# Kernel tuning notes

Measured on AMD Instinct MI355X. Metric: run time of the kernel, lower is better.

Reference implementation:

```python
import jax, jax.numpy as jnp
import numpy as np

B, N, E = 4, 4096, 1024
H, D = 16, 64          # num_heads, head_dim
K = 256                # proj_dim
MAXN = 4096
RANK = 32


def setup_inputs() -> dict:
    key = jax.random.key(0)
    ks = jax.random.split(key, 9)
    def w(k, shape, fan_in):
        return jax.random.normal(k, shape, jnp.float32) * (1.0 / np.sqrt(fan_in))
    return {
        "x": jax.random.normal(ks[0], (B, N, E), jnp.float32),
        "qU": w(ks[1], (RANK, E), E),            # LowRankLinear U: [rank, in]
        "qV": w(ks[2], (E // 2, RANK), RANK),    # LowRankLinear V: [out, rank]
        "qW": w(ks[3], (H * D, E // 2), E // 2), # final query Linear weight
        "qb": jnp.zeros((H * D,), jnp.float32),
        "kW": w(ks[4], (D, E), E),               # key_transform (single kv head)
        "key_proj": w(ks[5], (MAXN, K), MAXN),   # Linformer projection [max_seq_len, proj_dim]
        "oW": w(ks[6], (E, H * D), H * D),
        "ob": jnp.zeros((E,), jnp.float32),
    }


def reference(x, qU, qV, qW, qb, kW, key_proj, oW, ob):
    b, n, _ = x.shape
    # query: LowRankLinear then Linear
    q = ((x @ qU.T) @ qV.T) @ qW.T + qb              # [b, n, H*D]
    # shared single-head key/value, projected along sequence to K slots
    k = x @ kW.T                                     # [b, n, D]
    kv = jnp.einsum('bnd,nk->bkd', k, key_proj[:n])  # [b, K, D]
    q = q.reshape(b, n, H, D).transpose(0, 2, 1, 3)  # [b, H, n, D]
    kv = kv[:, None]                                 # [b, 1, K, D] broadcasts over heads
    scores = jnp.einsum('bhnd,bhkd->bhnk', q, kv) * (D ** -0.5)
    w = jax.nn.softmax(scores, axis=-1)              # [b, H, n, K]
    out = jnp.einsum('bhnk,bhkd->bhnd', w, kv)       # [b, H, n, D]
    out = out.transpose(0, 2, 1, 3).reshape(b, n, H * D)
    return out @ oW.T + ob
```

## Files before the change

### kernel.cpp

```cpp
#include <hip/hip_runtime.h>


typedef unsigned short u16;
typedef _Float16 f16;
typedef __attribute__((ext_vector_type(8))) _Float16 h8;
typedef __attribute__((ext_vector_type(4))) float f32x4;
typedef __attribute__((ext_vector_type(8))) unsigned short us8;
typedef __attribute__((ext_vector_type(4))) unsigned short us4;

__device__ __forceinline__ u16 f2h(float x) {
    f16 h = (f16)x;
    union { f16 hf; u16 u; } c; c.hf = h; return c.u;
}
__device__ __forceinline__ void async16(const void* g, void* l) {
    __builtin_amdgcn_global_load_lds(
        (const __attribute__((address_space(1))) void*)g,
        (__attribute__((address_space(3))) void*)l, 16, 0, 0);
}

__global__ __launch_bounds__(256)
void cvt_w(const float* __restrict__ src, u16* __restrict__ h, int n4) {
    int i = blockIdx.x * 256 + threadIdx.x;
    if (i >= n4) return;
    float4 v = ((const float4*)src)[i];
    u16 hh[4] = {f2h(v.x), f2h(v.y), f2h(v.z), f2h(v.w)};
    ((us4*)h)[i] = *(const us4*)hh;
}

template <bool HAS_BIAS, bool OUT_F16>
__global__ __launch_bounds__(256)
void gemm_ps(const u16* __restrict__ A_g, const u16* __restrict__ B_g,
             const float* __restrict__ bias, void* __restrict__ C_p,
             int M, int N, int K) {
    __shared__ u16 LA[128 * 32], LB[128 * 32];
    const int t = threadIdx.x;
    const int wave = t >> 6, lane = t & 63;
    const int l15 = lane & 15, quad = lane >> 4;
    const int wm = (wave >> 1) * 64, wn = (wave & 1) * 64;
    const int gx = gridDim.x;
    const int nwg = gx * gridDim.y;
    const int flat = blockIdx.y * gx + blockIdx.x;
    const int cpx = nwg >> 3;
    const int swz = (flat & 7) * cpx + (flat >> 3);
    const int m0 = (swz / gx) * 128, n0 = (swz % gx) * 128;
    const int rl = lane >> 2, c4 = lane & 3;

    f32x4 acc[4][4] = {};

    for (int k0 = 0; k0 < K; k0 += 32) {
#pragma unroll
        for (int j = 0; j < 2; ++j) {
            const int rloc = (wave * 2 + j) * 16 + rl;
            const size_t ga = (size_t)(m0 + rloc) * K + k0 + c4 * 8;
            const size_t gb = (size_t)(n0 + rloc) * K + k0 + c4 * 8;
            const int lo = (wave * 2 + j) * 512;
            async16(&A_g[ga], &LA[lo]);
            async16(&B_g[gb], &LB[lo]);
        }
        __syncthreads();

        h8 ah[4], bh[4];
#pragma unroll
        for (int i = 0; i < 4; ++i) {
            ah[i] = *(const h8*)&LA[(wm + i * 16 + l15) * 32 + quad * 8];
            bh[i] = *(const h8*)&LB[(wn + i * 16 + l15) * 32 + quad * 8];
        }
#pragma unroll
        for (int i = 0; i < 4; ++i)
#pragma unroll
            for (int j = 0; j < 4; ++j)
                acc[i][j] = __builtin_amdgcn_mfma_f32_16x16x32_f16(ah[i], bh[j], acc[i][j], 0, 0, 0);
        __syncthreads();
    }

#pragma unroll
    for (int j = 0; j < 4; ++j) {
        const int col = n0 + wn + j * 16 + l15;
        const float badd = HAS_BIAS ? bias[col] : 0.f;
#pragma unroll
        for (int i = 0; i < 4; ++i) {
            const int rbase = m0 + wm + i * 16 + quad * 4;
#pragma unroll
            for (int r = 0; r < 4; ++r) {
                float v = acc[i][j][r] + badd;
                size_t idx = (size_t)(rbase + r) * N + col;
                if (OUT_F16) ((u16*)C_p)[idx] = f2h(v);
                else         ((float*)C_p)[idx] = v;
            }
        }
    }
}

template <int BN, bool OUT_F16>
__global__ __launch_bounds__(256)
void gemm_xa(const float* __restrict__ A, const u16* __restrict__ B_g,
             void* __restrict__ C_p, int M, int N, int K) {
    constexpr int MI = (BN == 128) ? 4 : 2;
    constexpr int NJ = (BN == 32) ? 2 : 4;
    __shared__ u16 Ah[128][40], Bh[BN][40];
    const int t = threadIdx.x;
    const int wave = t >> 6, lane = t & 63;
    const int l15 = lane & 15, quad = lane >> 4;
    const int wm = (BN == 128) ? (wave >> 1) * 64 : wave * 32;
    const int wn = (BN == 128) ? (wave & 1) * 64 : 0;
    const int m0 = blockIdx.y * 128, n0 = blockIdx.x * BN;
    const int arow = t >> 1, acol = (t & 1) * 16;

    f32x4 acc[MI][NJ] = {};

    for (int k0 = 0; k0 < K; k0 += 32) {
        {
            const float* src = &A[(size_t)(m0 + arow) * K + k0 + acol];
            float4 w0 = ((const float4*)src)[0], w1 = ((const float4*)src)[1];
            float4 w2 = ((const float4*)src)[2], w3 = ((const float4*)src)[3];
            float v[16] = {w0.x, w0.y, w0.z, w0.w, w1.x, w1.y, w1.z, w1.w,
                           w2.x, w2.y, w2.z, w2.w, w3.x, w3.y, w3.z, w3.w};
            u16 hh[16];
#pragma unroll
            for (int e = 0; e < 16; ++e) hh[e] = f2h(v[e]);
            *(us8*)&Ah[arow][acol]     = *(const us8*)&hh[0];
            *(us8*)&Ah[arow][acol + 8] = *(const us8*)&hh[8];
        }
        if (t < BN * 2) {
            const int brow = t >> 1, bcol = (t & 1) * 16;
            size_t base = (size_t)(n0 + brow) * K + k0 + bcol;
            *(us8*)&Bh[brow][bcol]     = *(const us8*)&B_g[base];
            *(us8*)&Bh[brow][bcol + 8] = *(const us8*)&B_g[base + 8];
        }
        __syncthreads();

        h8 ah[MI], bh[NJ];
#pragma unroll
        for (int i = 0; i < MI; ++i)
            ah[i] = *(const h8*)&Ah[wm + i * 16 + l15][quad * 8];
#pragma unroll
        for (int j = 0; j < NJ; ++j)
            bh[j] = *(const h8*)&Bh[wn + j * 16 + l15][quad * 8];
#pragma unroll
        for (int i = 0; i < MI; ++i)
#pragma unroll
            for (int j = 0; j < NJ; ++j)
                acc[i][j] = __builtin_amdgcn_mfma_f32_16x16x32_f16(ah[i], bh[j], acc[i][j], 0, 0, 0);
        __syncthreads();
    }

#pragma unroll
    for (int j = 0; j < NJ; ++j) {
        const int col = n0 + wn + j * 16 + l15;
#pragma unroll
        for (int i = 0; i < MI; ++i) {
            const int rbase = m0 + wm + i * 16 + quad * 4;
#pragma unroll
            for (int r = 0; r < 4; ++r) {
                float v = acc[i][j][r];
                size_t idx = (size_t)(rbase + r) * N + col;
                if (OUT_F16) ((u16*)C_p)[idx] = f2h(v);
                else         ((float*)C_p)[idx] = v;
            }
        }
    }
}

__global__ __launch_bounds__(256)
void kv_partial(const float* __restrict__ kmat, const float* __restrict__ kp,
                float* __restrict__ part) {
    const int b = blockIdx.y;
    const int seg = blockIdx.z;
    const int kk0 = blockIdx.x * 16;
    const int tid = threadIdx.x;
    const int d = tid & 63, s = tid >> 6;

    float acc[16] = {};
    const int nbeg = seg * 512;
    for (int n = nbeg + s; n < nbeg + 512; n += 4) {
        const float kval = kmat[((size_t)b * 4096 + n) * 64 + d];
        const float* kpr = &kp[(size_t)n * 256 + kk0];
#pragma unroll
        for (int j = 0; j < 16; ++j) acc[j] += kval * kpr[j];
    }
    __shared__ float sm[16][4][64];
#pragma unroll
    for (int j = 0; j < 16; ++j) sm[j][s][d] = acc[j];
    __syncthreads();
    for (int o = tid; o < 16 * 64; o += 256) {
        const int j = o >> 6, dd = o & 63;
        part[(((size_t)seg * 4 + b) * 256 + kk0 + j) * 64 + dd] =
            sm[j][0][dd] + sm[j][1][dd] + sm[j][2][dd] + sm[j][3][dd];
    }
}

__global__ __launch_bounds__(256)
void kv_reduce_cvt(const float* __restrict__ part,
                   u16* __restrict__ kvh, u16* __restrict__ kvTh) {
    const int i = blockIdx.x * 256 + threadIdx.x;
    float s = 0.f;
#pragma unroll
    for (int seg = 0; seg < 8; ++seg) s += part[(size_t)seg * 65536 + i];
    u16 hh = f2h(s);
    kvh[i] = hh;
    const int b = i >> 14, k = (i >> 6) & 255, d = i & 63;
    kvTh[((size_t)b * 64 + d) * 256 + k] = hh;
}

__global__ __launch_bounds__(256)
void attn_fused(const u16* __restrict__ qh,
                const u16* __restrict__ kvh, const u16* __restrict__ kvTh,
                u16* __restrict__ ath) {
    __shared__ u16 Kh_s[64][72];
    __shared__ u16 Vh_s[64][72];
    __shared__ u16 Ps[128 * 64];
    const int b = blockIdx.z, h = blockIdx.y;
    const int t = threadIdx.x, wave = t >> 6, lane = t & 63;
    const int l15 = lane & 15, quad = lane >> 4;
    const int nblk = blockIdx.x * 128;
    const int nwav = wave * 32;
    char* Pb = (char*)Ps;

    h8 Qf[2][2];
#pragma unroll
    for (int nt = 0; nt < 2; ++nt) {
        size_t qoff = ((size_t)(b * 4096 + nblk + nwav + nt * 16 + l15)) * 1024
                      + h * 64 + quad * 8;
#pragma unroll
        for (int c = 0; c < 2; ++c)
            Qf[nt][c] = *(const h8*)&qh[qoff + c * 32];
    }

    f32x4 O[2][4] = {};
    float rsum[2] = {0.f, 0.f};

    const int srow = t >> 3;
    const int scol = (t & 7) * 8;
    const size_t kb = (size_t)b * 16384;

    for (int kc = 0; kc < 4; ++kc) {
        {
            us8 s0 = *(const us8*)&kvh [kb + (size_t)(kc * 64 + srow     ) * 64 + scol];
            us8 s1 = *(const us8*)&kvh [kb + (size_t)(kc * 64 + srow + 32) * 64 + scol];
            us8 s4 = *(const us8*)&kvTh[kb + (size_t)(srow     ) * 256 + kc * 64 + scol];
            us8 s5 = *(const us8*)&kvTh[kb + (size_t)(srow + 32) * 256 + kc * 64 + scol];
            *(us8*)&Kh_s[srow     ][scol] = s0;
            *(us8*)&Kh_s[srow + 32][scol] = s1;
            *(us8*)&Vh_s[srow     ][scol] = s4;
            *(us8*)&Vh_s[srow + 32][scol] = s5;
        }
        __syncthreads();

        f32x4 S[2][4] = {};
#pragma unroll
        for (int ktl = 0; ktl < 4; ++ktl) {
            const int krl = ktl * 16 + l15;
#pragma unroll
            for (int c = 0; c < 2; ++c) {
                h8 Kf = *(const h8*)&Kh_s[krl][c * 32 + quad * 8];
#pragma unroll
                for (int nt = 0; nt < 2; ++nt)
                    S[nt][ktl] = __builtin_amdgcn_mfma_f32_16x16x32_f16(Kf, Qf[nt][c], S[nt][ktl], 0, 0, 0);
            }
        }
#pragma unroll
        for (int nt = 0; nt < 2; ++nt) {
            const int nrel = nwav + nt * 16 + l15;
#pragma unroll
            for (int ktl = 0; ktl < 4; ++ktl) {
                u16 pw[4];
#pragma unroll
                for (int r = 0; r < 4; ++r) {
                    float p = __expf(S[nt][ktl][r] * 0.125f - 4.0f);
                    rsum[nt] += p;
                    pw[r] = f2h(p);
                }
                *(us4*)(Pb + ((nrel * 128 + ktl * 32 + quad * 8) ^ ((nrel & 7) << 4)))
                    = *(const us4*)pw;
            }
        }

#pragma unroll
        for (int c = 0; c < 2; ++c) {
            h8 pf[2];
#pragma unroll
            for (int nt = 0; nt < 2; ++nt) {
                const int nrel = nwav + nt * 16 + l15;
                pf[nt] = *(const h8*)(Pb + ((nrel * 128 + c * 64 + quad * 16) ^ ((nrel & 7) << 4)));
            }
#pragma unroll
            for (int dt = 0; dt < 4; ++dt) {
                const int drow = dt * 16 + l15;
                h8 th = *(const h8*)&Vh_s[drow][c * 32 + quad * 8];
#pragma unroll
                for (int nt = 0; nt < 2; ++nt)
                    O[nt][dt] = __builtin_amdgcn_mfma_f32_16x16x32_f16(pf[nt], th, O[nt][dt], 0, 0, 0);
            }
        }
        __syncthreads();
    }

    float inv[2];
#pragma unroll
    for (int nt = 0; nt < 2; ++nt) {
        float s = rsum[nt];
        s += __shfl_xor(s, 16, 64);
        s += __shfl_xor(s, 32, 64);
        inv[nt] = 1.f / s;
    }

#pragma unroll
    for (int nt = 0; nt < 2; ++nt)
#pragma unroll
        for (int dt = 0; dt < 4; ++dt) {
            const int dcol = dt * 16 + l15;
#pragma unroll
            for (int r = 0; r < 4; ++r) {
                const float qinv = __shfl(inv[nt], quad * 4 + r, 16);
                const int query = nblk + nwav + nt * 16 + quad * 4 + r;
                float v = O[nt][dt][r] * qinv;
                size_t idx = (size_t)(b * 4096 + query) * 1024 + h * 64 + dcol;
                ath[idx] = f2h(v);
            }
        }
}

extern "C" void kernel_launch(void* const* d_in, const int* in_sizes, int n_in,
                              void* d_out, int out_size, void* d_ws, size_t ws_size,
                              hipStream_t stream) {
    const float* x  = (const float*)d_in[0];
    const float* qU = (const float*)d_in[1];
    const float* qV = (const float*)d_in[2];
    const float* qW = (const float*)d_in[3];
    const float* qb = (const float*)d_in[4];
    const float* kW = (const float*)d_in[5];
    const float* kp = (const float*)d_in[6];
    const float* oW = (const float*)d_in[7];
    const float* ob = (const float*)d_in[8];
    float* out = (float*)d_out;

    const int M = 16384;
    u16* W = (u16*)d_ws;
    u16* qUh = W;  W += 32768;
    u16* qVh = W;  W += 16384;
    u16* qWh = W;  W += 524288;
    u16* kWh = W;  W += 65536;
    u16* oWh = W;  W += 1048576;
    u16* t1h = W;  W += 524288;
    u16* t2h = W;  W += 8388608;
    u16* qhb = W;  W += 16777216;
    float* km  = (float*)W;  W += 2097152;
    u16* kvh  = W;  W += 65536;
    u16* kvTh = W;  W += 65536;
    u16* ath = qhb;
    float* part = (float*)t2h;

    const dim3 blk(256);
    cvt_w<<<dim3(32),   blk, 0, stream>>>(qU, qUh, 8192);
    cvt_w<<<dim3(16),   blk, 0, stream>>>(qV, qVh, 4096);
    cvt_w<<<dim3(512),  blk, 0, stream>>>(qW, qWh, 131072);
    cvt_w<<<dim3(64),   blk, 0, stream>>>(kW, kWh, 16384);
    cvt_w<<<dim3(1024), blk, 0, stream>>>(oW, oWh, 262144);
    gemm_xa<32, true><<<dim3(1, 128), blk, 0, stream>>>(
        x, qUh, t1h, M, 32, 1024);
    gemm_ps<false, true><<<dim3(4, 128), blk, 0, stream>>>(
        t1h, qVh, nullptr, t2h, M, 512, 32);
    gemm_ps<true, true><<<dim3(8, 128), blk, 0, stream>>>(
        t2h, qWh, qb, qhb, M, 1024, 512);
    gemm_xa<64, false><<<dim3(1, 128), blk, 0, stream>>>(
        x, kWh, km, M, 64, 1024);
    kv_partial<<<dim3(16, 4, 8), blk, 0, stream>>>(km, kp, part);
    kv_reduce_cvt<<<dim3(256), blk, 0, stream>>>(part, kvh, kvTh);
    attn_fused<<<dim3(32, 16, 4), blk, 0, stream>>>(qhb, kvh, kvTh, ath);
    gemm_ps<true, false><<<dim3(8, 128), blk, 0, stream>>>(
        ath, oWh, ob, out, M, 1024, 1024);
}
```

Measured before the change: 377.1 us.

## Fold qV into qW and fuse x projections for query and key

Result: faster. 341.8 us (-9.3%).

```diff
diff --git a/kernel.cpp b/kernel.cpp
--- a/kernel.cpp
+++ b/kernel.cpp
@@ -25,6 +25,36 @@
     float4 v = ((const float4*)src)[i];
     u16 hh[4] = {f2h(v.x), f2h(v.y), f2h(v.z), f2h(v.w)};
     ((us4*)h)[i] = *(const us4*)hh;
+}
+
+__global__ __launch_bounds__(256)
+void wc_compute(const float* __restrict__ qW, const float* __restrict__ qV,
+                u16* __restrict__ Wc) {
+    __shared__ float Vs[128][32];
+    const int t = threadIdx.x;
+    const int nl = t >> 3;
+    const int rg = t & 7;
+    const int n0 = blockIdx.x * 32;
+    float acc[4] = {0.f, 0.f, 0.f, 0.f};
+    for (int e0 = 0; e0 < 512; e0 += 128) {
+#pragma unroll
+        for (int u = 0; u < 16; ++u) {
+            int idx = u * 256 + t;
+            int ee = idx >> 5, rr = idx & 31;
+            Vs[ee][rr] = qV[(size_t)(e0 + ee) * 32 + rr];
+        }
+        __syncthreads();
+        for (int e = 0; e < 128; ++e) {
+            float w = qW[(size_t)(n0 + nl) * 512 + e0 + e];
+#pragma unroll
+            for (int rr = 0; rr < 4; ++rr)
+                acc[rr] += w * Vs[e][rg * 4 + rr];
+        }
+        __syncthreads();
+    }
+#pragma unroll
+    for (int rr = 0; rr < 4; ++rr)
+        Wc[(size_t)(n0 + nl) * 32 + rg * 4 + rr] = f2h(acc[rr]);
 }
 
 template <bool HAS_BIAS, bool OUT_F16>
@@ -91,72 +121,58 @@
     }
 }
 
-template <int BN, bool OUT_F16>
-__global__ __launch_bounds__(256)
-void gemm_xa(const float* __restrict__ A, const u16* __restrict__ B_g,
-             void* __restrict__ C_p, int M, int N, int K) {
-    constexpr int MI = (BN == 128) ? 4 : 2;
-    constexpr int NJ = (BN == 32) ? 2 : 4;
-    __shared__ u16 Ah[128][40], Bh[BN][40];
+__global__ __launch_bounds__(256)
+void gemm_x96(const float* __restrict__ A, const u16* __restrict__ B_g,
+              u16* __restrict__ t1, float* __restrict__ km, int K) {
+    __shared__ u16 Ah[64][40], Bh[96][40];
     const int t = threadIdx.x;
     const int wave = t >> 6, lane = t & 63;
     const int l15 = lane & 15, quad = lane >> 4;
-    const int wm = (BN == 128) ? (wave >> 1) * 64 : wave * 32;
-    const int wn = (BN == 128) ? (wave & 1) * 64 : 0;
-    const int m0 = blockIdx.y * 128, n0 = blockIdx.x * BN;
-    const int arow = t >> 1, acol = (t & 1) * 16;
-
-    f32x4 acc[MI][NJ] = {};
+    const int wm = wave * 16;
+    const int m0 = blockIdx.y * 64;
+    const int arow = t >> 2, acol = (t & 3) * 8;
+
+    f32x4 acc[6] = {};
 
     for (int k0 = 0; k0 < K; k0 += 32) {
         {
             const float* src = &A[(size_t)(m0 + arow) * K + k0 + acol];
             float4 w0 = ((const float4*)src)[0], w1 = ((const float4*)src)[1];
-            float4 w2 = ((const float4*)src)[2], w3 = ((const float4*)src)[3];
-            float v[16] = {w0.x, w0.y, w0.z, w0.w, w1.x, w1.y, w1.z, w1.w,
-                           w2.x, w2.y, w2.z, w2.w, w3.x, w3.y, w3.z, w3.w};
-            u16 hh[16];
-#pragma unroll
-            for (int e = 0; e < 16; ++e) hh[e] = f2h(v[e]);
-            *(us8*)&Ah[arow][acol]     = *(const us8*)&hh[0];
-            *(us8*)&Ah[arow][acol + 8] = *(const us8*)&hh[8];
-        }
-        if (t < BN * 2) {
+            float v[8] = {w0.x, w0.y, w0.z, w0.w, w1.x, w1.y, w1.z, w1.w};
+            u16 hh[8];
+#pragma unroll
+            for (int e = 0; e < 8; ++e) hh[e] = f2h(v[e]);
+            *(us8*)&Ah[arow][acol] = *(const us8*)&hh[0];
+        }
+        if (t < 192) {
             const int brow = t >> 1, bcol = (t & 1) * 16;
-            size_t base = (size_t)(n0 + brow) * K + k0 + bcol;
+            size_t base = (size_t)brow * K + k0 + bcol;
             *(us8*)&Bh[brow][bcol]     = *(const us8*)&B_g[base];
             *(us8*)&Bh[brow][bcol + 8] = *(const us8*)&B_g[base + 8];
         }
         __syncthreads();
 
-        h8 ah[MI], bh[NJ];
-#pragma unroll
-        for (int i = 0; i < MI; ++i)
-            ah[i] = *(const h8*)&Ah[wm + i * 16 + l15][quad * 8];
-#pragma unroll
-        for (int j = 0; j < NJ; ++j)
-            bh[j] = *(const h8*)&Bh[wn + j * 16 + l15][quad * 8];
-#pragma unroll
-        for (int i = 0; i < MI; ++i)
-#pragma unroll
-            for (int j = 0; j < NJ; ++j)
-                acc[i][j] = __builtin_amdgcn_mfma_f32_16x16x32_f16(ah[i], bh[j], acc[i][j], 0, 0, 0);
-        __syncthreads();
-    }
-
-#pragma unroll
-    for (int j = 0; j < NJ; ++j) {
-        const int col = n0 + wn + j * 16 + l15;
-#pragma unroll
-        for (int i = 0; i < MI; ++i) {
-            const int rbase = m0 + wm + i * 16 + quad * 4;
-#pragma unroll
-            for (int r = 0; r < 4; ++r) {
-                float v = acc[i][j][r];
-                size_t idx = (size_t)(rbase + r) * N + col;
-                if (OUT_F16) ((u16*)C_p)[idx] = f2h(v);
-                else         ((float*)C_p)[idx] = v;
-            }
+        h8 ah = *(const h8*)&Ah[wm + l15][quad * 8];
+        h8 bh[6];
+#pragma unroll
+        for (int j = 0; j < 6; ++j)
+            bh[j] = *(const h8*)&Bh[j * 16 + l15][quad * 8];
+#pragma unroll
+        for (int j = 0; j < 6; ++j)
+            acc[j] = __builtin_amdgcn_mfma_f32_16x16x32_f16(ah, bh[j], acc[j], 0, 0, 0);
+        __syncthreads();
+    }
+
+#pragma unroll
+    for (int j = 0; j < 6; ++j) {
+        const int col96 = j * 16 + l15;
+        const int rbase = m0 + wm + quad * 4;
+#pragma unroll
+        for (int r = 0; r < 4; ++r) {
+            float v = acc[j][r];
+            const int row = rbase + r;
+            if (col96 < 32) t1[(size_t)row * 32 + col96] = f2h(v);
+            else            km[(size_t)row * 64 + (col96 - 32)] = v;
         }
     }
 }
@@ -336,36 +352,27 @@
 
     const int M = 16384;
     u16* W = (u16*)d_ws;
-    u16* qUh = W;  W += 32768;
-    u16* qVh = W;  W += 16384;
-    u16* qWh = W;  W += 524288;
-    u16* kWh = W;  W += 65536;
+    u16* bUK = W;  W += 98304;
     u16* oWh = W;  W += 1048576;
+    u16* WcH = W;  W += 32768;
     u16* t1h = W;  W += 524288;
-    u16* t2h = W;  W += 8388608;
     u16* qhb = W;  W += 16777216;
     float* km  = (float*)W;  W += 2097152;
+    float* part = (float*)W; W += 1048576;
     u16* kvh  = W;  W += 65536;
     u16* kvTh = W;  W += 65536;
     u16* ath = qhb;
-    float* part = (float*)t2h;
 
     const dim3 blk(256);
-    cvt_w<<<dim3(32),   blk, 0, stream>>>(qU, qUh, 8192);
-    cvt_w<<<dim3(16),   blk, 0, stream>>>(qV, qVh, 4096);
-    cvt_w<<<dim3(512),  blk, 0, stream>>>(qW, qWh, 131072);
-    cvt_w<<<dim3(64),   blk, 0, stream>>>(kW, kWh, 16384);
+    cvt_w<<<dim3(32),   blk, 0, stream>>>(qU, bUK, 8192);
+    cvt_w<<<dim3(64),   blk, 0, stream>>>(kW, bUK + 32768, 16384);
     cvt_w<<<dim3(1024), blk, 0, stream>>>(oW, oWh, 262144);
-    gemm_xa<32, true><<<dim3(1, 128), blk, 0, stream>>>(
-        x, qUh, t1h, M, 32, 1024);
-    gemm_ps<false, true><<<dim3(4, 128), blk, 0, stream>>>(
-        t1h, qVh, nullptr, t2h, M, 512, 32);
-    gemm_ps<true, true><<<dim3(8, 128), blk, 0, stream>>>(
-        t2h, qWh, qb, qhb, M, 1024, 512);
-    gemm_xa<64, false><<<dim3(1, 128), blk, 0, stream>>>(
-        x, kWh, km, M, 64, 1024);
+    wc_compute<<<dim3(32), blk, 0, stream>>>(qW, qV, WcH);
+    gemm_x96<<<dim3(1, 256), blk, 0, stream>>>(x, bUK, t1h, km, 1024);
     kv_partial<<<dim3(16, 4, 8), blk, 0, stream>>>(km, kp, part);
     kv_reduce_cvt<<<dim3(256), blk, 0, stream>>>(part, kvh, kvTh);
+    gemm_ps<true, true><<<dim3(8, 128), blk, 0, stream>>>(
+        t1h, WcH, qb, qhb, M, 1024, 32);
     attn_fused<<<dim3(32, 16, 4), blk, 0, stream>>>(qhb, kvh, kvTh, ath);
     gemm_ps<true, false><<<dim3(8, 128), blk, 0, stream>>>(
         ath, oWh, ob, out, M, 1024, 1024);
```
